# Kernel optimization log

Hardware: AMD Instinct MI355X
Metric: run time of the kernel (lower is better)

## Reference

```python
import jax, jax.numpy as jnp
import numpy as np

KERNEL_MUL = 2.0
KERNEL_NUM = 5


def _index_matrix(b: int) -> jnp.ndarray:
    # non-linear JMMD index matrix (linear=False)
    im = np.zeros((2 * b, 2 * b), dtype=np.float32)
    off = 1.0 / float(b * (b - 1))
    eye = np.eye(b, dtype=bool)
    im[:b, :b][~eye] = off
    im[b:, b:][~eye] = off
    im[:b, b:] = -1.0 / float(b * b)
    im[b:, :b] = -1.0 / float(b * b)
    return jnp.asarray(im)


def _gaussian_kernel(source, target):
    total = jnp.concatenate([source, target], axis=0)  # [2b, d]
    n = total.shape[0]
    sq = jnp.sum(total * total, axis=1)  # [2b]
    # pairwise squared L2 via Gram matrix (same math as expand/diff/sum)
    l2 = sq[:, None] + sq[None, :] - 2.0 * (total @ total.T)
    l2 = jnp.maximum(l2, 0.0)
    # bandwidth computed on detached distances (torch uses .data)
    bw = jax.lax.stop_gradient(jnp.sum(l2)) / float(n * n - n)
    bw = bw / (KERNEL_MUL ** (KERNEL_NUM // 2))
    k = jnp.zeros_like(l2)
    for i in range(KERNEL_NUM):
        k = k + jnp.exp(-l2 / (bw * (KERNEL_MUL ** i)))
    return k


def setup_inputs() -> dict:
    key = jax.random.key(0)
    k1, k2, k3, k4 = jax.random.split(key, 4)
    b, d1, d2 = 2048, 4096, 2048
    return {
        "z1_s": jax.random.normal(k1, (b, d1), dtype=jnp.float32),
        "z1_t": jax.random.normal(k2, (b, d1), dtype=jnp.float32),
        "z2_s": jax.random.normal(k3, (b, d2), dtype=jnp.float32),
        "z2_t": jax.random.normal(k4, (b, d2), dtype=jnp.float32),
    }


def reference(z1_s, z1_t, z2_s, z2_t):
    b = z1_s.shape[0]
    index_matrix = _index_matrix(b)  # [2b, 2b]
    kernel_matrix = _gaussian_kernel(z1_s, z1_t) * _gaussian_kernel(z2_s, z2_t)
    loss = jnp.sum(kernel_matrix * index_matrix) + 2.0 / float(b - 1)
    return loss
```

## Files before the change

kernel.cpp:

```cpp
#include <hip/hip_runtime.h>
#include <cstdint>

#define NTOT 4096
#define BHALF 2048
#define D1 4096
#define D2 2048
#define TT 32
#define NTILES 528

typedef __attribute__((ext_vector_type(4))) float f32x4;
typedef __attribute__((ext_vector_type(4))) int i32x4;
typedef __attribute__((ext_vector_type(8))) int i32x8;

__device__ __forceinline__ void glds16(const uint8_t* g, uint8_t* l) {
    __builtin_amdgcn_global_load_lds(
        (const __attribute__((address_space(1))) void*)(uintptr_t)g,
        (__attribute__((address_space(3))) void*)(uint32_t)(uintptr_t)l,
        16, 0, 0);
}

__device__ __forceinline__ i32x4 ldsr(uint32_t addr) {
    i32x4 r;
    asm volatile("ds_read_b128 %0, %1" : "=v"(r) : "v"(addr));
    return r;
}

__device__ __forceinline__ float fp8dec(unsigned b) {
    unsigned e = (b >> 3) & 15u, m = b & 7u;
    float v = e ? __uint_as_float(((e + 120u) << 23) | (m << 20))
                : (float)m * 0.001953125f;
    return (b & 128u) ? -v : v;
}

__global__ void prep_kernel(const float* __restrict__ z1s, const float* __restrict__ z1t,
                            const float* __restrict__ z2s, const float* __restrict__ z2t,
                            float* __restrict__ sq1, float* __restrict__ sq2,
                            uint8_t* __restrict__ t1f8, uint8_t* __restrict__ t2f8,
                            float* __restrict__ s1, float* __restrict__ s2) {
    int bid = blockIdx.x;
    int tid = threadIdx.x;
    if (bid == 0) { for (int i = tid; i < 4096; i += 256) s1[i] = 0.f; }
    if (bid == 1) { for (int i = tid; i < 2048; i += 256) s2[i] = 0.f; }
    int which = bid >> 12;
    int row = bid & 4095;
    int d = which ? D2 : D1;
    const float* s_ = which ? z2s : z1s;
    const float* t_ = which ? z2t : z1t;
    const float* src = (row < BHALF) ? s_ + (size_t)row * d : t_ + (size_t)(row - BHALF) * d;
    uint8_t* dst = (which ? t2f8 : t1f8) + (size_t)row * d;
    float* sq = which ? sq2 : sq1;
    const float4* src4 = (const float4*)src;
    float a = 0.f;
    int n8 = d >> 3;
    for (int i = tid; i < n8; i += 256) {
        float4 v0 = src4[2 * i], v1 = src4[2 * i + 1];
        a += v0.x * v0.x + v0.y * v0.y + v0.z * v0.z + v0.w * v0.w;
        a += v1.x * v1.x + v1.y * v1.y + v1.z * v1.z + v1.w * v1.w;
        int w0 = __builtin_amdgcn_cvt_pk_fp8_f32(v0.x, v0.y, 0, 0);
        w0 = __builtin_amdgcn_cvt_pk_fp8_f32(v0.z, v0.w, w0, 1);
        int w1 = __builtin_amdgcn_cvt_pk_fp8_f32(v1.x, v1.y, 0, 0);
        w1 = __builtin_amdgcn_cvt_pk_fp8_f32(v1.z, v1.w, w1, 1);
        ((uint2*)dst)[i] = uint2{(unsigned)w0, (unsigned)w1};
    }
    for (int o = 32; o; o >>= 1) a += __shfl_down(a, o);
    __shared__ float sh[4];
    int lane = tid & 63, w = tid >> 6;
    if (lane == 0) sh[w] = a;
    __syncthreads();
    if (tid == 0) sq[row] = sh[0] + sh[1] + sh[2] + sh[3];
}

__global__ void colsum_fp8_kernel(const uint8_t* __restrict__ t1f8,
                                  const uint8_t* __restrict__ t2f8,
                                  float* __restrict__ s1, float* __restrict__ s2) {
    int bid = blockIdx.x;
    int which = bid >= 256;
    int local = which ? bid - 256 : bid;
    int d = which ? D2 : D1;
    int colchunks = d >> 10;
    int cb = local % colchunks, rb = local / colchunks;
    const uint8_t* base = which ? t2f8 : t1f8;
    float* s = which ? s2 : s1;
    int col = (cb << 10) + threadIdx.x * 4;
    int r0 = rb * 64;
    float a0 = 0.f, a1 = 0.f, a2 = 0.f, a3 = 0.f;
    const uint8_t* p = base + (size_t)r0 * d + col;
#pragma unroll 4
    for (int r = 0; r < 64; ++r) {
        uchar4 u = *(const uchar4*)(p + (size_t)r * d);
        a0 += fp8dec(u.x); a1 += fp8dec(u.y); a2 += fp8dec(u.z); a3 += fp8dec(u.w);
    }
    atomicAdd(&s[col], a0); atomicAdd(&s[col + 1], a1);
    atomicAdd(&s[col + 2], a2); atomicAdd(&s[col + 3], a3);
}

__global__ void finalize_kernel(const float* __restrict__ s1, const float* __restrict__ s2,
                                const float* __restrict__ sq1, const float* __restrict__ sq2,
                                float* __restrict__ acc, float* __restrict__ out) {
    int tid = threadIdx.x;
    float a1 = 0.f, a2 = 0.f, q1 = 0.f, q2 = 0.f;
    for (int i = tid; i < 4096; i += 256) { float v = s1[i]; a1 += v * v; q1 += sq1[i]; q2 += sq2[i]; }
    for (int i = tid; i < 2048; i += 256) { float v = s2[i]; a2 += v * v; }
    for (int o = 32; o; o >>= 1) {
        a1 += __shfl_down(a1, o); a2 += __shfl_down(a2, o);
        q1 += __shfl_down(q1, o); q2 += __shfl_down(q2, o);
    }
    __shared__ float sh[4][4];
    int lane = tid & 63, w = tid >> 6;
    if (lane == 0) { sh[0][w] = a1; sh[1][w] = a2; sh[2][w] = q1; sh[3][w] = q2; }
    __syncthreads();
    if (tid == 0) {
        double ss1 = (double)sh[0][0] + sh[0][1] + sh[0][2] + sh[0][3];
        double ss2 = (double)sh[1][0] + sh[1][1] + sh[1][2] + sh[1][3];
        double t1 = (double)sh[2][0] + sh[2][1] + sh[2][2] + sh[2][3];
        double t2 = (double)sh[3][0] + sh[3][1] + sh[3][2] + sh[3][3];
        double S1 = 2.0 * (double)NTOT * t1 - 2.0 * ss1;
        double S2 = 2.0 * (double)NTOT * t2 - 2.0 * ss2;
        const double L2E = 1.4426950408889634;
        double nn = (double)NTOT * (double)(NTOT - 1);
        acc[2] = (float)(nn * L2E / (4.0 * S1));
        acc[3] = (float)(nn * L2E / (4.0 * S2));
        out[0] = 2.0f / (float)(BHALF - 1);
    }
}

__device__ __forceinline__ void gemm_mx_pipe(const uint8_t* __restrict__ ga,
                                             const uint8_t* __restrict__ gb,
                                             int d,
                                             uint8_t* A0, uint8_t* B0,
                                             uint8_t* A1, uint8_t* B1,
                                             f32x4 (&acc)[4][4], int wv, int lane,
                                             int wm, int wn, int lm, int quad) {
    int nsteps = d >> 7;
    int rsub = lane >> 3;
    int ql = (lane & 7) ^ rsub;
    const uint8_t* pa = ga + (size_t)(wv * 32 + rsub) * d + ql * 16;
    const uint8_t* pb = gb + (size_t)(wv * 32 + rsub) * d + ql * 16;
    uint8_t* dA[2] = { A0 + wv * 4096, A1 + wv * 4096 };
    uint8_t* dB[2] = { B0 + wv * 4096, B1 + wv * 4096 };
    uint32_t baseA[2] = { (uint32_t)(uintptr_t)A0, (uint32_t)(uintptr_t)A1 };
    uint32_t baseB[2] = { (uint32_t)(uintptr_t)B0, (uint32_t)(uintptr_t)B1 };
    int s0 = ((2 * quad) ^ (lm & 7)) * 16;
    int s1 = ((2 * quad + 1) ^ (lm & 7)) * 16;
    uint32_t offA[4], offB[4];
#pragma unroll
    for (int i = 0; i < 4; ++i) {
        offA[i] = (uint32_t)((wm * 64 + i * 16 + lm) * 128);
        offB[i] = (uint32_t)((wn * 64 + i * 16 + lm) * 128);
    }
#pragma unroll
    for (int i = 0; i < 4; ++i) {
        glds16(pa + (size_t)i * 8 * d, dA[0] + i * 1024);
        glds16(pb + (size_t)i * 8 * d, dB[0] + i * 1024);
    }
    for (int k = 0; k < nsteps; ++k) {
        int cur = k & 1, nxt = cur ^ 1;
        size_t koff = (size_t)((k + 1 < nsteps) ? (k + 1) : 0) << 7;
#pragma unroll
        for (int i = 0; i < 4; ++i) {
            glds16(pa + koff + (size_t)i * 8 * d, dA[nxt] + i * 1024);
            glds16(pb + koff + (size_t)i * 8 * d, dB[nxt] + i * 1024);
        }
        asm volatile("s_waitcnt vmcnt(8)\n\ts_barrier" ::: "memory");
        i32x4 b00 = ldsr(baseB[cur] + offB[0] + s0), b01 = ldsr(baseB[cur] + offB[0] + s1);
        i32x4 b10 = ldsr(baseB[cur] + offB[1] + s0), b11 = ldsr(baseB[cur] + offB[1] + s1);
        i32x4 a00 = ldsr(baseA[cur] + offA[0] + s0), a01 = ldsr(baseA[cur] + offA[0] + s1);
        i32x4 a10 = ldsr(baseA[cur] + offA[1] + s0), a11 = ldsr(baseA[cur] + offA[1] + s1);
        i32x4 b20 = ldsr(baseB[cur] + offB[2] + s0), b21 = ldsr(baseB[cur] + offB[2] + s1);
        i32x4 b30 = ldsr(baseB[cur] + offB[3] + s0), b31 = ldsr(baseB[cur] + offB[3] + s1);
        i32x4 a20 = ldsr(baseA[cur] + offA[2] + s0), a21 = ldsr(baseA[cur] + offA[2] + s1);
        i32x4 a30 = ldsr(baseA[cur] + offA[3] + s0), a31 = ldsr(baseA[cur] + offA[3] + s1);
        union F { i32x4 h[2]; i32x8 v; };
        F ua0, ua1, ua2, ua3, ub0, ub1, ub2, ub3;
        asm volatile("s_waitcnt lgkmcnt(8)"
                     : "+v"(b00), "+v"(b01), "+v"(b10), "+v"(b11),
                       "+v"(a00), "+v"(a01), "+v"(a10), "+v"(a11));
        __builtin_amdgcn_sched_barrier(0);
        ub0.h[0] = b00; ub0.h[1] = b01; ub1.h[0] = b10; ub1.h[1] = b11;
        ua0.h[0] = a00; ua0.h[1] = a01; ua1.h[0] = a10; ua1.h[1] = a11;
        __builtin_amdgcn_s_setprio(1);
        acc[0][0] = __builtin_amdgcn_mfma_scale_f32_16x16x128_f8f6f4(ua0.v, ub0.v, acc[0][0], 0, 0, 0, 0x7F7F7F7F, 0, 0x7F7F7F7F);
        acc[0][1] = __builtin_amdgcn_mfma_scale_f32_16x16x128_f8f6f4(ua0.v, ub1.v, acc[0][1], 0, 0, 0, 0x7F7F7F7F, 0, 0x7F7F7F7F);
        acc[1][0] = __builtin_amdgcn_mfma_scale_f32_16x16x128_f8f6f4(ua1.v, ub0.v, acc[1][0], 0, 0, 0, 0x7F7F7F7F, 0, 0x7F7F7F7F);
        acc[1][1] = __builtin_amdgcn_mfma_scale_f32_16x16x128_f8f6f4(ua1.v, ub1.v, acc[1][1], 0, 0, 0, 0x7F7F7F7F, 0, 0x7F7F7F7F);
        __builtin_amdgcn_s_setprio(0);
        asm volatile("s_waitcnt lgkmcnt(4)"
                     : "+v"(b20), "+v"(b21), "+v"(b30), "+v"(b31));
        __builtin_amdgcn_sched_barrier(0);
        ub2.h[0] = b20; ub2.h[1] = b21; ub3.h[0] = b30; ub3.h[1] = b31;
        __builtin_amdgcn_s_setprio(1);
        acc[0][2] = __builtin_amdgcn_mfma_scale_f32_16x16x128_f8f6f4(ua0.v, ub2.v, acc[0][2], 0, 0, 0, 0x7F7F7F7F, 0, 0x7F7F7F7F);
        acc[0][3] = __builtin_amdgcn_mfma_scale_f32_16x16x128_f8f6f4(ua0.v, ub3.v, acc[0][3], 0, 0, 0, 0x7F7F7F7F, 0, 0x7F7F7F7F);
        acc[1][2] = __builtin_amdgcn_mfma_scale_f32_16x16x128_f8f6f4(ua1.v, ub2.v, acc[1][2], 0, 0, 0, 0x7F7F7F7F, 0, 0x7F7F7F7F);
        acc[1][3] = __builtin_amdgcn_mfma_scale_f32_16x16x128_f8f6f4(ua1.v, ub3.v, acc[1][3], 0, 0, 0, 0x7F7F7F7F, 0, 0x7F7F7F7F);
        __builtin_amdgcn_s_setprio(0);
        asm volatile("s_waitcnt lgkmcnt(0)"
                     : "+v"(a20), "+v"(a21), "+v"(a30), "+v"(a31));
        __builtin_amdgcn_sched_barrier(0);
        asm volatile("s_barrier" ::: "memory");
        __builtin_amdgcn_sched_barrier(0);
        ua2.h[0] = a20; ua2.h[1] = a21; ua3.h[0] = a30; ua3.h[1] = a31;
        __builtin_amdgcn_s_setprio(1);
        acc[2][0] = __builtin_amdgcn_mfma_scale_f32_16x16x128_f8f6f4(ua2.v, ub0.v, acc[2][0], 0, 0, 0, 0x7F7F7F7F, 0, 0x7F7F7F7F);
        acc[2][1] = __builtin_amdgcn_mfma_scale_f32_16x16x128_f8f6f4(ua2.v, ub1.v, acc[2][1], 0, 0, 0, 0x7F7F7F7F, 0, 0x7F7F7F7F);
        acc[2][2] = __builtin_amdgcn_mfma_scale_f32_16x16x128_f8f6f4(ua2.v, ub2.v, acc[2][2], 0, 0, 0, 0x7F7F7F7F, 0, 0x7F7F7F7F);
        acc[2][3] = __builtin_amdgcn_mfma_scale_f32_16x16x128_f8f6f4(ua2.v, ub3.v, acc[2][3], 0, 0, 0, 0x7F7F7F7F, 0, 0x7F7F7F7F);
        acc[3][0] = __builtin_amdgcn_mfma_scale_f32_16x16x128_f8f6f4(ua3.v, ub0.v, acc[3][0], 0, 0, 0, 0x7F7F7F7F, 0, 0x7F7F7F7F);
        acc[3][1] = __builtin_amdgcn_mfma_scale_f32_16x16x128_f8f6f4(ua3.v, ub1.v, acc[3][1], 0, 0, 0, 0x7F7F7F7F, 0, 0x7F7F7F7F);
        acc[3][2] = __builtin_amdgcn_mfma_scale_f32_16x16x128_f8f6f4(ua3.v, ub2.v, acc[3][2], 0, 0, 0, 0x7F7F7F7F, 0, 0x7F7F7F7F);
        acc[3][3] = __builtin_amdgcn_mfma_scale_f32_16x16x128_f8f6f4(ua3.v, ub3.v, acc[3][3], 0, 0, 0, 0x7F7F7F7F, 0, 0x7F7F7F7F);
        __builtin_amdgcn_s_setprio(0);
    }
}

__global__ __launch_bounds__(256, 2) void jmmd_fused(
    const uint8_t* __restrict__ t1f8, const uint8_t* __restrict__ t2f8,
    const float* __restrict__ sq1, const float* __restrict__ sq2,
    const float* __restrict__ cv, float* __restrict__ out) {
    __shared__ alignas(16) uint8_t smem[4][16384];
    int tid = threadIdx.x;
    int ti = 0, r = blockIdx.x;
    while (r >= TT - ti) { r -= TT - ti; ++ti; }
    int tj = ti + r;
    int i0 = ti * 128, j0 = tj * 128;
    int lane = tid & 63, wv = tid >> 6;
    int wm = wv >> 1, wn = wv & 1, lm = lane & 15, quad = lane >> 4;
    f32x4 acc1[4][4] = {};
    f32x4 acc2[4][4] = {};
    gemm_mx_pipe(t1f8 + (size_t)i0 * D1, t1f8 + (size_t)j0 * D1, D1,
                 smem[0], smem[1], smem[2], smem[3], acc1, wv, lane, wm, wn, lm, quad);
    asm volatile("s_waitcnt vmcnt(0)\n\ts_barrier" ::: "memory");
    gemm_mx_pipe(t2f8 + (size_t)i0 * D2, t2f8 + (size_t)j0 * D2, D2,
                 smem[0], smem[1], smem[2], smem[3], acc2, wv, lane, wm, wn, lm, quad);
    asm volatile("s_waitcnt vmcnt(0)" ::: "memory");
    __syncthreads();
    float c1 = cv[0], c2 = cv[1];
    float local = 0.f;
    bool diag = (ti == tj);
#pragma unroll
    for (int mi = 0; mi < 4; ++mi) {
        int rbase = wm * 64 + mi * 16 + quad * 4;
#pragma unroll
        for (int ni = 0; ni < 4; ++ni) {
            int col = wn * 64 + ni * 16 + lm;
            float sb1 = sq1[j0 + col], sb2 = sq2[j0 + col];
#pragma unroll
            for (int rr = 0; rr < 4; ++rr) {
                int row = rbase + rr;
                float l2a = fmaxf(sq1[i0 + row] + sb1 - 2.f * acc1[mi][ni][rr], 0.f);
                float l2b = fmaxf(sq2[i0 + row] + sb2 - 2.f * acc2[mi][ni][rr], 0.f);
                float t1 = __builtin_amdgcn_exp2f(-l2a * c1);
                float k1 = t1; float u1 = t1 * t1; k1 += u1; u1 *= u1; k1 += u1; u1 *= u1; k1 += u1; u1 *= u1; k1 += u1;
                float t2 = __builtin_amdgcn_exp2f(-l2b * c2);
                float k2 = t2; float u2 = t2 * t2; k2 += u2; u2 *= u2; k2 += u2; u2 *= u2; k2 += u2; u2 *= u2; k2 += u2;
                float v = k1 * k2;
                if (diag && (row == col)) v = 0.f;
                local += v;
            }
        }
    }
    for (int o = 32; o; o >>= 1) local += __shfl_down(local, o);
    float* redp = (float*)smem[0];
    if (lane == 0) redp[wv] = local;
    __syncthreads();
    if (tid == 0) {
        bool same = (i0 < BHALF) == (j0 < BHALF);
        float w = same ? (1.0f / ((float)BHALF * (float)(BHALF - 1)))
                       : (-1.0f / ((float)BHALF * (float)BHALF));
        if (!diag) w *= 2.f;
        atomicAdd(out, (redp[0] + redp[1] + redp[2] + redp[3]) * w);
    }
}

extern "C" void kernel_launch(void* const* d_in, const int* in_sizes, int n_in,
                              void* d_out, int out_size, void* d_ws, size_t ws_size,
                              hipStream_t stream) {
    const float* z1s = (const float*)d_in[0];
    const float* z1t = (const float*)d_in[1];
    const float* z2s = (const float*)d_in[2];
    const float* z2t = (const float*)d_in[3];
    float* out = (float*)d_out;

    float* ws = (float*)d_ws;
    float* sq1 = ws;
    float* sq2 = ws + 4096;
    float* s1  = ws + 8192;
    float* s2  = ws + 12288;
    float* acc = ws + 14336;
    uint8_t* t1f8 = (uint8_t*)(ws + 14344);
    uint8_t* t2f8 = t1f8 + (size_t)NTOT * D1;

    prep_kernel<<<8192, 256, 0, stream>>>(z1s, z1t, z2s, z2t, sq1, sq2, t1f8, t2f8, s1, s2);
    colsum_fp8_kernel<<<384, 256, 0, stream>>>(t1f8, t2f8, s1, s2);
    finalize_kernel<<<1, 256, 0, stream>>>(s1, s2, sq1, sq2, acc, out);
    jmmd_fused<<<NTILES, 256, 0, stream>>>(t1f8, t2f8, sq1, sq2, acc + 2, out);
}
```

Before: 270.7 us.

## Fuse column-sum and bandwidth finalize into GEMM kernel via grid-wide flag

Removes the separate colsum and finalize launches. The first 384 blocks of the fused GEMM kernel compute the fp8 column sums, and the last block to finish, found through an atomic counter, computes the bandwidth constants and publishes them through a ready flag. Every block then runs its GEMM tiles and spin-waits on that flag only before the exp epilogue, so the reduction overlaps with the matrix work and two launch gaps disappear. This relies on the 384 reduction blocks being resident or finishing before the waiting blocks starve them, which holds only if all blocks fit on the device at once.

```diff
diff --git a/kernel.cpp b/kernel.cpp
--- a/kernel.cpp
+++ b/kernel.cpp
@@ -36,11 +36,16 @@
                             const float* __restrict__ z2s, const float* __restrict__ z2t,
                             float* __restrict__ sq1, float* __restrict__ sq2,
                             uint8_t* __restrict__ t1f8, uint8_t* __restrict__ t2f8,
-                            float* __restrict__ s1, float* __restrict__ s2) {
+                            float* __restrict__ s1, float* __restrict__ s2,
+                            unsigned* __restrict__ ctrl, float* __restrict__ out) {
     int bid = blockIdx.x;
     int tid = threadIdx.x;
     if (bid == 0) { for (int i = tid; i < 4096; i += 256) s1[i] = 0.f; }
     if (bid == 1) { for (int i = tid; i < 2048; i += 256) s2[i] = 0.f; }
+    if (bid == 2) {
+        if (tid < 4) ctrl[tid] = 0u;
+        if (tid == 4) out[0] = 2.0f / (float)(BHALF - 1);
+    }
     int which = bid >> 12;
     int row = bid & 4095;
     int d = which ? D2 : D1;
@@ -68,60 +73,6 @@
     if (lane == 0) sh[w] = a;
     __syncthreads();
     if (tid == 0) sq[row] = sh[0] + sh[1] + sh[2] + sh[3];
-}
-
-__global__ void colsum_fp8_kernel(const uint8_t* __restrict__ t1f8,
-                                  const uint8_t* __restrict__ t2f8,
-                                  float* __restrict__ s1, float* __restrict__ s2) {
-    int bid = blockIdx.x;
-    int which = bid >= 256;
-    int local = which ? bid - 256 : bid;
-    int d = which ? D2 : D1;
-    int colchunks = d >> 10;
-    int cb = local % colchunks, rb = local / colchunks;
-    const uint8_t* base = which ? t2f8 : t1f8;
-    float* s = which ? s2 : s1;
-    int col = (cb << 10) + threadIdx.x * 4;
-    int r0 = rb * 64;
-    float a0 = 0.f, a1 = 0.f, a2 = 0.f, a3 = 0.f;
-    const uint8_t* p = base + (size_t)r0 * d + col;
-#pragma unroll 4
-    for (int r = 0; r < 64; ++r) {
-        uchar4 u = *(const uchar4*)(p + (size_t)r * d);
-        a0 += fp8dec(u.x); a1 += fp8dec(u.y); a2 += fp8dec(u.z); a3 += fp8dec(u.w);
-    }
-    atomicAdd(&s[col], a0); atomicAdd(&s[col + 1], a1);
-    atomicAdd(&s[col + 2], a2); atomicAdd(&s[col + 3], a3);
-}
-
-__global__ void finalize_kernel(const float* __restrict__ s1, const float* __restrict__ s2,
-                                const float* __restrict__ sq1, const float* __restrict__ sq2,
-                                float* __restrict__ acc, float* __restrict__ out) {
-    int tid = threadIdx.x;
-    float a1 = 0.f, a2 = 0.f, q1 = 0.f, q2 = 0.f;
-    for (int i = tid; i < 4096; i += 256) { float v = s1[i]; a1 += v * v; q1 += sq1[i]; q2 += sq2[i]; }
-    for (int i = tid; i < 2048; i += 256) { float v = s2[i]; a2 += v * v; }
-    for (int o = 32; o; o >>= 1) {
-        a1 += __shfl_down(a1, o); a2 += __shfl_down(a2, o);
-        q1 += __shfl_down(q1, o); q2 += __shfl_down(q2, o);
-    }
-    __shared__ float sh[4][4];
-    int lane = tid & 63, w = tid >> 6;
-    if (lane == 0) { sh[0][w] = a1; sh[1][w] = a2; sh[2][w] = q1; sh[3][w] = q2; }
-    __syncthreads();
-    if (tid == 0) {
-        double ss1 = (double)sh[0][0] + sh[0][1] + sh[0][2] + sh[0][3];
-        double ss2 = (double)sh[1][0] + sh[1][1] + sh[1][2] + sh[1][3];
-        double t1 = (double)sh[2][0] + sh[2][1] + sh[2][2] + sh[2][3];
-        double t2 = (double)sh[3][0] + sh[3][1] + sh[3][2] + sh[3][3];
-        double S1 = 2.0 * (double)NTOT * t1 - 2.0 * ss1;
-        double S2 = 2.0 * (double)NTOT * t2 - 2.0 * ss2;
-        const double L2E = 1.4426950408889634;
-        double nn = (double)NTOT * (double)(NTOT - 1);
-        acc[2] = (float)(nn * L2E / (4.0 * S1));
-        acc[3] = (float)(nn * L2E / (4.0 * S2));
-        out[0] = 2.0f / (float)(BHALF - 1);
-    }
 }
 
 __device__ __forceinline__ void gemm_mx_pipe(const uint8_t* __restrict__ ga,
@@ -216,10 +167,74 @@
 __global__ __launch_bounds__(256, 2) void jmmd_fused(
     const uint8_t* __restrict__ t1f8, const uint8_t* __restrict__ t2f8,
     const float* __restrict__ sq1, const float* __restrict__ sq2,
-    const float* __restrict__ cv, float* __restrict__ out) {
+    float* __restrict__ s1v, float* __restrict__ s2v,
+    unsigned* __restrict__ ctrl, float* __restrict__ out) {
     __shared__ alignas(16) uint8_t smem[4][16384];
     int tid = threadIdx.x;
-    int ti = 0, r = blockIdx.x;
+    int bid = blockIdx.x;
+
+    if (bid < 384) {
+        int which = bid >= 256;
+        int local = which ? bid - 256 : bid;
+        int d = which ? D2 : D1;
+        int colchunks = d >> 10;
+        int cb = local % colchunks, rb = local / colchunks;
+        const uint8_t* base = which ? t2f8 : t1f8;
+        float* s = which ? s2v : s1v;
+        int col = (cb << 10) + tid * 4;
+        const uint8_t* p = base + (size_t)(rb * 64) * d + col;
+        float a0 = 0.f, a1 = 0.f, a2 = 0.f, a3 = 0.f;
+#pragma unroll 4
+        for (int r = 0; r < 64; ++r) {
+            uchar4 u = *(const uchar4*)(p + (size_t)r * d);
+            a0 += fp8dec(u.x); a1 += fp8dec(u.y); a2 += fp8dec(u.z); a3 += fp8dec(u.w);
+        }
+        atomicAdd(&s[col], a0); atomicAdd(&s[col + 1], a1);
+        atomicAdd(&s[col + 2], a2); atomicAdd(&s[col + 3], a3);
+        __threadfence();
+        __syncthreads();
+        unsigned* rkp = (unsigned*)(smem[0] + 64);
+        if (tid == 0) *rkp = atomicAdd(&ctrl[0], 1u);
+        __syncthreads();
+        unsigned rk = *rkp;
+        __syncthreads();
+        if (rk == 383u) {
+            float a1_ = 0.f, a2_ = 0.f, q1_ = 0.f, q2_ = 0.f;
+            for (int i = tid; i < 4096; i += 256) {
+                float v = __uint_as_float(atomicOr((unsigned*)&s1v[i], 0u));
+                a1_ += v * v; q1_ += sq1[i]; q2_ += sq2[i];
+            }
+            for (int i = tid; i < 2048; i += 256) {
+                float v = __uint_as_float(atomicOr((unsigned*)&s2v[i], 0u));
+                a2_ += v * v;
+            }
+            for (int o = 32; o; o >>= 1) {
+                a1_ += __shfl_down(a1_, o); a2_ += __shfl_down(a2_, o);
+                q1_ += __shfl_down(q1_, o); q2_ += __shfl_down(q2_, o);
+            }
+            float* fsh = (float*)smem[0];
+            int lane = tid & 63, w = tid >> 6;
+            if (lane == 0) { fsh[0 * 4 + w] = a1_; fsh[1 * 4 + w] = a2_; fsh[2 * 4 + w] = q1_; fsh[3 * 4 + w] = q2_; }
+            __syncthreads();
+            if (tid == 0) {
+                double ss1 = (double)fsh[0] + fsh[1] + fsh[2] + fsh[3];
+                double ss2 = (double)fsh[4] + fsh[5] + fsh[6] + fsh[7];
+                double t1 = (double)fsh[8] + fsh[9] + fsh[10] + fsh[11];
+                double t2 = (double)fsh[12] + fsh[13] + fsh[14] + fsh[15];
+                double S1 = 2.0 * (double)NTOT * t1 - 2.0 * ss1;
+                double S2 = 2.0 * (double)NTOT * t2 - 2.0 * ss2;
+                const double L2E = 1.4426950408889634;
+                double nn = (double)NTOT * (double)(NTOT - 1);
+                atomicExch(&ctrl[2], __float_as_uint((float)(nn * L2E / (4.0 * S1))));
+                atomicExch(&ctrl[3], __float_as_uint((float)(nn * L2E / (4.0 * S2))));
+                __threadfence();
+                atomicExch(&ctrl[1], 1u);
+            }
+            __syncthreads();
+        }
+    }
+
+    int ti = 0, r = bid;
     while (r >= TT - ti) { r -= TT - ti; ++ti; }
     int tj = ti + r;
     int i0 = ti * 128, j0 = tj * 128;
@@ -234,7 +249,15 @@
                  smem[0], smem[1], smem[2], smem[3], acc2, wv, lane, wm, wn, lm, quad);
     asm volatile("s_waitcnt vmcnt(0)" ::: "memory");
     __syncthreads();
-    float c1 = cv[0], c2 = cv[1];
+
+    float* cvp = (float*)smem[1];
+    if (tid == 0) {
+        while (atomicOr(&ctrl[1], 0u) == 0u) __builtin_amdgcn_s_sleep(8);
+        cvp[0] = __uint_as_float(atomicOr(&ctrl[2], 0u));
+        cvp[1] = __uint_as_float(atomicOr(&ctrl[3], 0u));
+    }
+    __syncthreads();
+    float c1 = cvp[0], c2 = cvp[1];
     float local = 0.f;
     bool diag = (ti == tj);
 #pragma unroll
@@ -286,12 +309,10 @@
     float* sq2 = ws + 4096;
     float* s1  = ws + 8192;
     float* s2  = ws + 12288;
-    float* acc = ws + 14336;
+    unsigned* ctrl = (unsigned*)(ws + 14336);
     uint8_t* t1f8 = (uint8_t*)(ws + 14344);
     uint8_t* t2f8 = t1f8 + (size_t)NTOT * D1;
 
-    prep_kernel<<<8192, 256, 0, stream>>>(z1s, z1t, z2s, z2t, sq1, sq2, t1f8, t2f8, s1, s2);
-    colsum_fp8_kernel<<<384, 256, 0, stream>>>(t1f8, t2f8, s1, s2);
-    finalize_kernel<<<1, 256, 0, stream>>>(s1, s2, sq1, sq2, acc, out);
-    jmmd_fused<<<NTILES, 256, 0, stream>>>(t1f8, t2f8, sq1, sq2, acc + 2, out);
-}
+    prep_kernel<<<8192, 256, 0, stream>>>(z1s, z1t, z2s, z2t, sq1, sq2, t1f8, t2f8, s1, s2, ctrl, out);
+    jmmd_fused<<<NTILES, 256, 0, stream>>>(t1f8, t2f8, sq1, sq2, s1, s2, ctrl, out);
+}
```

Result: slower. 296.6 us (+9.6%).

## Single-buffer B tile to cut LDS and raise occupancy to three blocks

Applied to the files above, without the earlier changes.

The B operand tile is no longer double-buffered: it is loaded into one LDS buffer at the start of each k-step, while A stays double-buffered and is prefetched. This drops LDS use from 64KB to 48KB per block, and launch bounds are raised to 3 blocks per CU. The B load latency is now exposed inside each iteration, so it must be hidden by the extra resident blocks. Register pressure rises under the tighter launch bound, which may cause spills.

```diff
diff --git a/kernel.cpp b/kernel.cpp
--- a/kernel.cpp
+++ b/kernel.cpp
@@ -127,8 +127,7 @@
 __device__ __forceinline__ void gemm_mx_pipe(const uint8_t* __restrict__ ga,
                                              const uint8_t* __restrict__ gb,
                                              int d,
-                                             uint8_t* A0, uint8_t* B0,
-                                             uint8_t* A1, uint8_t* B1,
+                                             uint8_t* A0, uint8_t* A1, uint8_t* B,
                                              f32x4 (&acc)[4][4], int wv, int lane,
                                              int wm, int wn, int lm, int quad) {
     int nsteps = d >> 7;
@@ -137,9 +136,9 @@
     const uint8_t* pa = ga + (size_t)(wv * 32 + rsub) * d + ql * 16;
     const uint8_t* pb = gb + (size_t)(wv * 32 + rsub) * d + ql * 16;
     uint8_t* dA[2] = { A0 + wv * 4096, A1 + wv * 4096 };
-    uint8_t* dB[2] = { B0 + wv * 4096, B1 + wv * 4096 };
+    uint8_t* dB = B + wv * 4096;
     uint32_t baseA[2] = { (uint32_t)(uintptr_t)A0, (uint32_t)(uintptr_t)A1 };
-    uint32_t baseB[2] = { (uint32_t)(uintptr_t)B0, (uint32_t)(uintptr_t)B1 };
+    uint32_t baseB = (uint32_t)(uintptr_t)B;
     int s0 = ((2 * quad) ^ (lm & 7)) * 16;
     int s1 = ((2 * quad + 1) ^ (lm & 7)) * 16;
     uint32_t offA[4], offB[4];
@@ -149,25 +148,22 @@
         offB[i] = (uint32_t)((wn * 64 + i * 16 + lm) * 128);
     }
 #pragma unroll
-    for (int i = 0; i < 4; ++i) {
-        glds16(pa + (size_t)i * 8 * d, dA[0] + i * 1024);
-        glds16(pb + (size_t)i * 8 * d, dB[0] + i * 1024);
-    }
+    for (int i = 0; i < 4; ++i) glds16(pa + (size_t)i * 8 * d, dA[0] + i * 1024);
     for (int k = 0; k < nsteps; ++k) {
         int cur = k & 1, nxt = cur ^ 1;
+        size_t kb = (size_t)k << 7;
         size_t koff = (size_t)((k + 1 < nsteps) ? (k + 1) : 0) << 7;
 #pragma unroll
-        for (int i = 0; i < 4; ++i) {
-            glds16(pa + koff + (size_t)i * 8 * d, dA[nxt] + i * 1024);
-            glds16(pb + koff + (size_t)i * 8 * d, dB[nxt] + i * 1024);
-        }
-        asm volatile("s_waitcnt vmcnt(8)\n\ts_barrier" ::: "memory");
-        i32x4 b00 = ldsr(baseB[cur] + offB[0] + s0), b01 = ldsr(baseB[cur] + offB[0] + s1);
-        i32x4 b10 = ldsr(baseB[cur] + offB[1] + s0), b11 = ldsr(baseB[cur] + offB[1] + s1);
+        for (int i = 0; i < 4; ++i) glds16(pb + kb + (size_t)i * 8 * d, dB + i * 1024);
+#pragma unroll
+        for (int i = 0; i < 4; ++i) glds16(pa + koff + (size_t)i * 8 * d, dA[nxt] + i * 1024);
+        asm volatile("s_waitcnt vmcnt(4)\n\ts_barrier" ::: "memory");
+        i32x4 b00 = ldsr(baseB + offB[0] + s0), b01 = ldsr(baseB + offB[0] + s1);
+        i32x4 b10 = ldsr(baseB + offB[1] + s0), b11 = ldsr(baseB + offB[1] + s1);
         i32x4 a00 = ldsr(baseA[cur] + offA[0] + s0), a01 = ldsr(baseA[cur] + offA[0] + s1);
         i32x4 a10 = ldsr(baseA[cur] + offA[1] + s0), a11 = ldsr(baseA[cur] + offA[1] + s1);
-        i32x4 b20 = ldsr(baseB[cur] + offB[2] + s0), b21 = ldsr(baseB[cur] + offB[2] + s1);
-        i32x4 b30 = ldsr(baseB[cur] + offB[3] + s0), b31 = ldsr(baseB[cur] + offB[3] + s1);
+        i32x4 b20 = ldsr(baseB + offB[2] + s0), b21 = ldsr(baseB + offB[2] + s1);
+        i32x4 b30 = ldsr(baseB + offB[3] + s0), b31 = ldsr(baseB + offB[3] + s1);
         i32x4 a20 = ldsr(baseA[cur] + offA[2] + s0), a21 = ldsr(baseA[cur] + offA[2] + s1);
         i32x4 a30 = ldsr(baseA[cur] + offA[3] + s0), a31 = ldsr(baseA[cur] + offA[3] + s1);
         union F { i32x4 h[2]; i32x8 v; };
@@ -213,11 +209,11 @@
     }
 }
 
-__global__ __launch_bounds__(256, 2) void jmmd_fused(
+__global__ __launch_bounds__(256, 3) void jmmd_fused(
     const uint8_t* __restrict__ t1f8, const uint8_t* __restrict__ t2f8,
     const float* __restrict__ sq1, const float* __restrict__ sq2,
     const float* __restrict__ cv, float* __restrict__ out) {
-    __shared__ alignas(16) uint8_t smem[4][16384];
+    __shared__ alignas(16) uint8_t smem[3][16384];
     int tid = threadIdx.x;
     int ti = 0, r = blockIdx.x;
     while (r >= TT - ti) { r -= TT - ti; ++ti; }
@@ -228,10 +224,10 @@
     f32x4 acc1[4][4] = {};
     f32x4 acc2[4][4] = {};
     gemm_mx_pipe(t1f8 + (size_t)i0 * D1, t1f8 + (size_t)j0 * D1, D1,
-                 smem[0], smem[1], smem[2], smem[3], acc1, wv, lane, wm, wn, lm, quad);
+                 smem[0], smem[1], smem[2], acc1, wv, lane, wm, wn, lm, quad);
     asm volatile("s_waitcnt vmcnt(0)\n\ts_barrier" ::: "memory");
     gemm_mx_pipe(t2f8 + (size_t)i0 * D2, t2f8 + (size_t)j0 * D2, D2,
-                 smem[0], smem[1], smem[2], smem[3], acc2, wv, lane, wm, wn, lm, quad);
+                 smem[0], smem[1], smem[2], acc2, wv, lane, wm, wn, lm, quad);
     asm volatile("s_waitcnt vmcnt(0)" ::: "memory");
     __syncthreads();
     float c1 = cv[0], c2 = cv[1];
```

Result: slower. 299.7 us (+10.7%).

## Split-K the leftover tiles across the first blocks to remove the tail wave

Applied to the files above, without the earlier changes.

The grid shrinks from 528 to 512 tile blocks, which should fit in a single wave at two blocks per CU. The 16 remaining tiles are split along K into 8 chunks each. The first 128 blocks compute those chunks before their own tile and atomically add the partial Gram products into zeroed global buffers. The last block to finish each leftover tile, tracked by a counter, runs the exp/weight epilogue for it. This trades a second, mostly idle wave for extra atomic traffic, buffer zeroing in prep and slightly longer runtimes for the first 128 blocks.

```diff
diff --git a/kernel.cpp b/kernel.cpp
--- a/kernel.cpp
+++ b/kernel.cpp
@@ -7,6 +7,8 @@
 #define D2 2048
 #define TT 32
 #define NTILES 528
+#define NMAIN 512
+#define NLEFT 16
 
 typedef __attribute__((ext_vector_type(4))) float f32x4;
 typedef __attribute__((ext_vector_type(4))) int i32x4;
@@ -36,11 +38,17 @@
                             const float* __restrict__ z2s, const float* __restrict__ z2t,
                             float* __restrict__ sq1, float* __restrict__ sq2,
                             uint8_t* __restrict__ t1f8, uint8_t* __restrict__ t2f8,
-                            float* __restrict__ s1, float* __restrict__ s2) {
+                            float* __restrict__ s1, float* __restrict__ s2,
+                            float* __restrict__ gpz, unsigned* __restrict__ ctrs) {
     int bid = blockIdx.x;
     int tid = threadIdx.x;
     if (bid == 0) { for (int i = tid; i < 4096; i += 256) s1[i] = 0.f; }
     if (bid == 1) { for (int i = tid; i < 2048; i += 256) s2[i] = 0.f; }
+    if (bid >= 3 && bid < 3 + 512) {
+        float4 z4 = float4{0.f, 0.f, 0.f, 0.f};
+        ((float4*)(gpz + (size_t)(bid - 3) * 1024))[tid] = z4;
+        if (bid == 3 && tid < NLEFT) ctrs[tid] = 0u;
+    }
     int which = bid >> 12;
     int row = bid & 4095;
     int d = which ? D2 : D1;
@@ -126,16 +134,15 @@
 
 __device__ __forceinline__ void gemm_mx_pipe(const uint8_t* __restrict__ ga,
                                              const uint8_t* __restrict__ gb,
-                                             int d,
+                                             int d, int kstart, int nsteps,
                                              uint8_t* A0, uint8_t* B0,
                                              uint8_t* A1, uint8_t* B1,
                                              f32x4 (&acc)[4][4], int wv, int lane,
                                              int wm, int wn, int lm, int quad) {
-    int nsteps = d >> 7;
     int rsub = lane >> 3;
     int ql = (lane & 7) ^ rsub;
-    const uint8_t* pa = ga + (size_t)(wv * 32 + rsub) * d + ql * 16;
-    const uint8_t* pb = gb + (size_t)(wv * 32 + rsub) * d + ql * 16;
+    const uint8_t* pa = ga + (size_t)(wv * 32 + rsub) * d + ql * 16 + ((size_t)kstart << 7);
+    const uint8_t* pb = gb + (size_t)(wv * 32 + rsub) * d + ql * 16 + ((size_t)kstart << 7);
     uint8_t* dA[2] = { A0 + wv * 4096, A1 + wv * 4096 };
     uint8_t* dB[2] = { B0 + wv * 4096, B1 + wv * 4096 };
     uint32_t baseA[2] = { (uint32_t)(uintptr_t)A0, (uint32_t)(uintptr_t)A1 };
@@ -213,24 +220,102 @@
     }
 }
 
+__device__ __forceinline__ void tile_from_index(int idx, int& ti, int& tj) {
+    int t = 0, r = idx;
+    while (r >= TT - t) { r -= TT - t; ++t; }
+    ti = t; tj = t + r;
+}
+
 __global__ __launch_bounds__(256, 2) void jmmd_fused(
     const uint8_t* __restrict__ t1f8, const uint8_t* __restrict__ t2f8,
     const float* __restrict__ sq1, const float* __restrict__ sq2,
-    const float* __restrict__ cv, float* __restrict__ out) {
+    const float* __restrict__ cv, float* __restrict__ gp1, float* __restrict__ gp2,
+    unsigned* __restrict__ ctrs, float* __restrict__ out) {
     __shared__ alignas(16) uint8_t smem[4][16384];
+    __shared__ float red2[4];
+    __shared__ unsigned done_sh;
     int tid = threadIdx.x;
-    int ti = 0, r = blockIdx.x;
-    while (r >= TT - ti) { r -= TT - ti; ++ti; }
-    int tj = ti + r;
-    int i0 = ti * 128, j0 = tj * 128;
+    int bid = blockIdx.x;
     int lane = tid & 63, wv = tid >> 6;
     int wm = wv >> 1, wn = wv & 1, lm = lane & 15, quad = lane >> 4;
+
+    if (bid < 8 * NLEFT) {
+        int lt = bid >> 3;
+        int c = bid & 7;
+        int cti, ctj;
+        tile_from_index(NMAIN + lt, cti, ctj);
+        int ci0 = cti * 128, cj0 = ctj * 128;
+        f32x4 p1[4][4] = {};
+        f32x4 p2[4][4] = {};
+        gemm_mx_pipe(t1f8 + (size_t)ci0 * D1, t1f8 + (size_t)cj0 * D1, D1, c * 4, 4,
+                     smem[0], smem[1], smem[2], smem[3], p1, wv, lane, wm, wn, lm, quad);
+        asm volatile("s_waitcnt vmcnt(0)\n\ts_barrier" ::: "memory");
+        gemm_mx_pipe(t2f8 + (size_t)ci0 * D2, t2f8 + (size_t)cj0 * D2, D2, c * 2, 2,
+                     smem[0], smem[1], smem[2], smem[3], p2, wv, lane, wm, wn, lm, quad);
+        asm volatile("s_waitcnt vmcnt(0)" ::: "memory");
+        __syncthreads();
+        float* g1 = gp1 + (size_t)lt * 16384;
+        float* g2 = gp2 + (size_t)lt * 16384;
+#pragma unroll
+        for (int mi = 0; mi < 4; ++mi) {
+            int rbase = wm * 64 + mi * 16 + quad * 4;
+#pragma unroll
+            for (int ni = 0; ni < 4; ++ni) {
+                int col = wn * 64 + ni * 16 + lm;
+#pragma unroll
+                for (int rr = 0; rr < 4; ++rr) {
+                    int idx = (rbase + rr) * 128 + col;
+                    atomicAdd(&g1[idx], p1[mi][ni][rr]);
+                    atomicAdd(&g2[idx], p2[mi][ni][rr]);
+                }
+            }
+        }
+        __threadfence();
+        __syncthreads();
+        if (tid == 0) done_sh = atomicAdd(&ctrs[lt], 1u);
+        __syncthreads();
+        if (done_sh == 7u) {
+            __threadfence();
+            float c1 = cv[0], c2 = cv[1];
+            bool cdiag = (cti == ctj);
+            float local = 0.f;
+            for (int idx = tid; idx < 16384; idx += 256) {
+                int row = idx >> 7, col = idx & 127;
+                float g1v = __uint_as_float(atomicOr((unsigned*)&g1[idx], 0u));
+                float g2v = __uint_as_float(atomicOr((unsigned*)&g2[idx], 0u));
+                float l2a = fmaxf(sq1[ci0 + row] + sq1[cj0 + col] - 2.f * g1v, 0.f);
+                float l2b = fmaxf(sq2[ci0 + row] + sq2[cj0 + col] - 2.f * g2v, 0.f);
+                float t1 = __builtin_amdgcn_exp2f(-l2a * c1);
+                float k1 = t1; float u1 = t1 * t1; k1 += u1; u1 *= u1; k1 += u1; u1 *= u1; k1 += u1; u1 *= u1; k1 += u1;
+                float t2 = __builtin_amdgcn_exp2f(-l2b * c2);
+                float k2 = t2; float u2 = t2 * t2; k2 += u2; u2 *= u2; k2 += u2; u2 *= u2; k2 += u2; u2 *= u2; k2 += u2;
+                float v = k1 * k2;
+                if (cdiag && (row == col)) v = 0.f;
+                local += v;
+            }
+            for (int o = 32; o; o >>= 1) local += __shfl_down(local, o);
+            if (lane == 0) red2[wv] = local;
+            __syncthreads();
+            if (tid == 0) {
+                bool same = (ci0 < BHALF) == (cj0 < BHALF);
+                float w = same ? (1.0f / ((float)BHALF * (float)(BHALF - 1)))
+                               : (-1.0f / ((float)BHALF * (float)BHALF));
+                if (!cdiag) w *= 2.f;
+                atomicAdd(out, (red2[0] + red2[1] + red2[2] + red2[3]) * w);
+            }
+            __syncthreads();
+        }
+    }
+
+    int ti, tj;
+    tile_from_index(bid, ti, tj);
+    int i0 = ti * 128, j0 = tj * 128;
     f32x4 acc1[4][4] = {};
     f32x4 acc2[4][4] = {};
-    gemm_mx_pipe(t1f8 + (size_t)i0 * D1, t1f8 + (size_t)j0 * D1, D1,
+    gemm_mx_pipe(t1f8 + (size_t)i0 * D1, t1f8 + (size_t)j0 * D1, D1, 0, D1 >> 7,
                  smem[0], smem[1], smem[2], smem[3], acc1, wv, lane, wm, wn, lm, quad);
     asm volatile("s_waitcnt vmcnt(0)\n\ts_barrier" ::: "memory");
-    gemm_mx_pipe(t2f8 + (size_t)i0 * D2, t2f8 + (size_t)j0 * D2, D2,
+    gemm_mx_pipe(t2f8 + (size_t)i0 * D2, t2f8 + (size_t)j0 * D2, D2, 0, D2 >> 7,
                  smem[0], smem[1], smem[2], smem[3], acc2, wv, lane, wm, wn, lm, quad);
     asm volatile("s_waitcnt vmcnt(0)" ::: "memory");
     __syncthreads();
@@ -289,9 +374,13 @@
     float* acc = ws + 14336;
     uint8_t* t1f8 = (uint8_t*)(ws + 14344);
     uint8_t* t2f8 = t1f8 + (size_t)NTOT * D1;
-
-    prep_kernel<<<8192, 256, 0, stream>>>(z1s, z1t, z2s, z2t, sq1, sq2, t1f8, t2f8, s1, s2);
+    float* gp1 = (float*)(t2f8 + (size_t)NTOT * D2);
+    float* gp2 = gp1 + (size_t)NLEFT * 16384;
+    unsigned* ctrs = (unsigned*)(gp2 + (size_t)NLEFT * 16384);
+
+    prep_kernel<<<8192, 256, 0, stream>>>(z1s, z1t, z2s, z2t, sq1, sq2, t1f8, t2f8,
+                                          s1, s2, gp1, ctrs);
     colsum_fp8_kernel<<<384, 256, 0, stream>>>(t1f8, t2f8, s1, s2);
     finalize_kernel<<<1, 256, 0, stream>>>(s1, s2, sq1, sq2, acc, out);
-    jmmd_fused<<<NTILES, 256, 0, stream>>>(t1f8, t2f8, sq1, sq2, acc + 2, out);
-}
+    jmmd_fused<<<NMAIN, 256, 0, stream>>>(t1f8, t2f8, sq1, sq2, acc + 2, gp1, gp2, ctrs, out);
+}
```

Result: slower. 308.9 us (+14.1%).
